# Optimization experiments

Measured on AMD Instinct MI355X. Metric: run time of the kernel, lower is better.

## Reference

```python
import jax, jax.numpy as jnp
import numpy as np

N = 50000      # nodes
E = 800000     # edges
H = 4          # heads (all layers)
D = 64         # per-head out dim (n_hidden == n_classes == 64)
IN = 256       # in_feats; also H*D so identity residual is valid
NEG_SLOPE = 0.2


def setup_inputs() -> dict:
    key = jax.random.key(0)
    ks = jax.random.split(key, 16)
    x = jax.random.normal(ks[0], (N, IN), dtype=jnp.float32)
    src = jax.random.randint(ks[1], (E,), 0, N, dtype=jnp.int32)
    dst = jax.random.randint(ks[2], (E,), 0, N, dtype=jnp.int32)
    inp = {"x": x, "src": src, "dst": dst}
    fan_ins = [IN, H * D, H * D]  # layer input widths
    for i, fin in enumerate(fan_ins):
        s = 1.0 / np.sqrt(fin)
        inp[f"W{i}"] = jax.random.normal(ks[3 + 4 * i], (fin, H * D), dtype=jnp.float32) * s
        inp[f"al{i}"] = jax.random.normal(ks[4 + 4 * i], (H, D), dtype=jnp.float32) * s
        inp[f"ar{i}"] = jax.random.normal(ks[5 + 4 * i], (H, D), dtype=jnp.float32) * s
        inp[f"b{i}"] = jnp.zeros((H * D,), dtype=jnp.float32)
    return inp


def _gat_layer(h, src, dst, W, al, ar, b, residual, activate):
    # project: [N, in] @ [in, H*D] -> [N, H, D]
    feat = (h @ W).reshape(-1, H, D)
    el = jnp.sum(feat * al, axis=-1)            # [N, H]
    er = jnp.sum(feat * ar, axis=-1)            # [N, H]
    e = jax.nn.leaky_relu(el[src] + er[dst], NEG_SLOPE)  # [E, H]
    # edge softmax per destination node (stable: subtract per-dst max)
    emax = jax.ops.segment_max(e, dst, num_segments=N)  # [N, H]
    e = jnp.exp(e - emax[dst])
    denom = jax.ops.segment_sum(e, dst, num_segments=N)  # [N, H]
    alpha = e / denom[dst]                               # [E, H]
    # message + scatter-aggregate: [E, H, D] summed into [N, H, D]
    out = jax.ops.segment_sum(alpha[:, :, None] * feat[src], dst, num_segments=N)
    if residual:
        out = out + h.reshape(-1, H, D)  # identity residual (in == H*D)
    out = out + b.reshape(1, H, D)
    if activate:
        out = jax.nn.elu(out)
    return out


def reference(x, src, dst, W0, al0, ar0, b0, W1, al1, ar1, b1, W2, al2, ar2, b2):
    h = _gat_layer(x, src, dst, W0, al0, ar0, b0, False, True).reshape(N, H * D)
    h = _gat_layer(h, src, dst, W1, al1, ar1, b1, True, True).reshape(N, H * D)
    h = _gat_layer(h, src, dst, W2, al2, ar2, b2, True, False).mean(axis=1)  # [N, D]
    return h
```

## Files before the change

kernel.cpp:

```cpp
#include <hip/hip_runtime.h>
#include <math.h>

#define N_NODES 50000
#define N_EDGES 800000
#define HD 256
#define NHEAD 4
#define DH 64
#define NPAD 50048

#define GEMM_BLKS 782
#define PACK_BLKS 96
#define EDGE_BLKS 1563
#define NB 49

typedef short bf16x8 __attribute__((ext_vector_type(8)));
typedef float f32x4 __attribute__((ext_vector_type(4)));

__device__ __forceinline__ unsigned short f2bf(float f) {
    unsigned u = __float_as_uint(f);
    return (unsigned short)((u + 0x7fffu + ((u >> 16) & 1u)) >> 16);
}
__device__ __forceinline__ float bf2f(unsigned short h) {
    return __uint_as_float((unsigned)h << 16);
}
__device__ __forceinline__ int origk(int k) {
    return (k & ~63) | ((k & 3) * 16 + ((k >> 2) & 15));
}

__device__ __forceinline__ void mfma_tile(const unsigned short* Asl,
                                          const unsigned short* wbase,
                                          int lane, f32x4 acc[4][4]) {
#pragma unroll
    for (int kk = 0; kk < 8; kk++) {
        bf16x8 a[4], b[4];
#pragma unroll
        for (int m = 0; m < 4; m++) {
            int r = m * 16 + (lane & 15);
            int kb = kk * 32 + (lane >> 4) * 8;
            int byt = (r * 512 + kb * 2) ^ ((r & 7) << 4);
            a[m] = *(const bf16x8*)((const char*)Asl + byt);
        }
#pragma unroll
        for (int n = 0; n < 4; n++)
            b[n] = *(const bf16x8*)(wbase + ((size_t)(n * 8 + kk) * 64 + lane) * 8);
#pragma unroll
        for (int m = 0; m < 4; m++)
#pragma unroll
            for (int n = 0; n < 4; n++)
                acc[m][n] = __builtin_amdgcn_mfma_f32_16x16x32_bf16(a[m], b[n],
                                                                    acc[m][n], 0, 0, 0);
    }
}

__device__ __forceinline__ void epilogue_tile(f32x4 acc[4][4], int bm, int wv, int lane,
                                              const float* __restrict__ al,
                                              const float* __restrict__ ar,
                                              unsigned short* __restrict__ C,
                                              unsigned short* __restrict__ el,
                                              float* __restrict__ er, int M) {
    int rr = lane >> 4, cc = lane & 15;
    float alv[4], arv[4];
#pragma unroll
    for (int n = 0; n < 4; n++) {
        alv[n] = al[wv * 64 + n * 16 + cc];
        arv[n] = ar[wv * 64 + n * 16 + cc];
    }
    float vl[16], vr[16];
#pragma unroll
    for (int m = 0; m < 4; m++)
#pragma unroll
        for (int r = 0; r < 4; r++) {
            float ep = 0.f, rp = 0.f;
#pragma unroll
            for (int n = 0; n < 4; n++) {
                ep = fmaf(acc[m][n][r], alv[n], ep);
                rp = fmaf(acc[m][n][r], arv[n], rp);
            }
            vl[m * 4 + r] = ep;
            vr[m * 4 + r] = rp;
        }
    float l8[8], r8[8];
#pragma unroll
    for (int i = 0; i < 8; i++) {
        float xs = (cc & 1) ? vl[2 * i] : vl[2 * i + 1];
        float xk = (cc & 1) ? vl[2 * i + 1] : vl[2 * i];
        l8[i] = xk + __shfl_xor(xs, 1);
        float ys = (cc & 1) ? vr[2 * i] : vr[2 * i + 1];
        float yk = (cc & 1) ? vr[2 * i + 1] : vr[2 * i];
        r8[i] = yk + __shfl_xor(ys, 1);
    }
    float l4[4], r4[4];
#pragma unroll
    for (int i = 0; i < 4; i++) {
        float xs = (cc & 2) ? l8[2 * i] : l8[2 * i + 1];
        float xk = (cc & 2) ? l8[2 * i + 1] : l8[2 * i];
        l4[i] = xk + __shfl_xor(xs, 2);
        float ys = (cc & 2) ? r8[2 * i] : r8[2 * i + 1];
        float yk = (cc & 2) ? r8[2 * i + 1] : r8[2 * i];
        r4[i] = yk + __shfl_xor(ys, 2);
    }
    float l2[2], r2[2];
#pragma unroll
    for (int i = 0; i < 2; i++) {
        float xs = (cc & 4) ? l4[2 * i] : l4[2 * i + 1];
        float xk = (cc & 4) ? l4[2 * i + 1] : l4[2 * i];
        l2[i] = xk + __shfl_xor(xs, 4);
        float ys = (cc & 4) ? r4[2 * i] : r4[2 * i + 1];
        float yk = (cc & 4) ? r4[2 * i + 1] : r4[2 * i];
        r2[i] = yk + __shfl_xor(ys, 4);
    }
    {
        float xs = (cc & 8) ? l2[0] : l2[1];
        float xk = (cc & 8) ? l2[1] : l2[0];
        float lv = xk + __shfl_xor(xs, 8);
        float ys = (cc & 8) ? r2[0] : r2[1];
        float yk = (cc & 8) ? r2[1] : r2[0];
        float rv = yk + __shfl_xor(ys, 8);
        int row_e = bm + (cc >> 2) * 16 + rr * 4 + (cc & 3);
        if (row_e < M) {
            el[(size_t)row_e * NHEAD + wv] = f2bf(lv);
            er[(size_t)row_e * NHEAD + wv] = rv;
        }
    }
#pragma unroll
    for (int m = 0; m < 4; m++) {
#pragma unroll
        for (int r = 0; r < 4; r++) {
            int row = bm + m * 16 + rr * 4 + r;
            if (row < M) {
                unsigned short p4[4] = {f2bf(acc[m][0][r]), f2bf(acc[m][1][r]),
                                        f2bf(acc[m][2][r]), f2bf(acc[m][3][r])};
                *(ushort4*)(C + (size_t)row * 256 + wv * 64 + cc * 4) = *(ushort4*)p4;
            }
        }
    }
}

__global__ __launch_bounds__(256) void fused_ph_k(const float* __restrict__ W0,
                                                  const float* __restrict__ W1,
                                                  const float* __restrict__ W2,
                                                  unsigned short* __restrict__ Wp,
                                                  const int* __restrict__ dst,
                                                  int* __restrict__ deg,
                                                  int* __restrict__ rank) {
    int blk = blockIdx.x, tid = threadIdx.x, wv = tid >> 6, lane = tid & 63;
    if (blk < PACK_BLKS) {
        int tile = blk * 4 + wv;
        int L = tile >> 7, t = tile & 127;
        const float* W = L == 0 ? W0 : L == 1 ? W1 : W2;
        int nt = t >> 3, kt = t & 7;
        int col = nt * 16 + (lane & 15);
        int kb = kt * 32 + (lane >> 4) * 8;
        unsigned short v[8];
#pragma unroll
        for (int j = 0; j < 8; j++) {
            int k = kb + j;
            if (L > 0) k = origk(k);
            v[j] = f2bf(W[(size_t)k * 256 + col]);
        }
        *(bf16x8*)(Wp + ((size_t)(L * 128 + t) * 64 + lane) * 8) = *(bf16x8*)v;
    } else {
        int t = (blk - PACK_BLKS) * 256 + tid;
        int e = t * 2;
        int* mydeg = deg + (size_t)(tid & 3) * NPAD;
        if (e + 1 < N_EDGES) {
            int2 d2 = *(const int2*)(dst + e);
            int r0 = atomicAdd(&mydeg[d2.x], 1);
            int r1 = atomicAdd(&mydeg[d2.y], 1);
            *(int2*)(rank + e) = make_int2(r0, r1);
        } else if (e < N_EDGES) {
            rank[e] = atomicAdd(&mydeg[dst[e]], 1);
        }
    }
}

__global__ __launch_bounds__(256) void scan1_k(const int* __restrict__ deg,
                                               int* __restrict__ rowptr,
                                               int* __restrict__ bsum,
                                               int* __restrict__ cpyoff) {
    __shared__ int wsum2[4];
    int tid = threadIdx.x, lane = tid & 63, wv = tid >> 6;
    int i0 = blockIdx.x * 1024 + tid * 4;
    int v[4], p[4];
#pragma unroll
    for (int j = 0; j < 4; j++) {
        int i = i0 + j;
        if (i < N_NODES) {
            int c0 = deg[i], c1 = deg[i + NPAD];
            int c2 = deg[i + 2 * NPAD], c3 = deg[i + 3 * NPAD];
            v[j] = c0 + c1 + c2 + c3;
            cpyoff[i] = 0;
            cpyoff[i + NPAD] = c0;
            cpyoff[i + 2 * NPAD] = c0 + c1;
            cpyoff[i + 3 * NPAD] = c0 + c1 + c2;
        } else {
            v[j] = 0;
        }
    }
    p[0] = v[0]; p[1] = p[0] + v[1]; p[2] = p[1] + v[2]; p[3] = p[2] + v[3];
    int tot = p[3];
    int sc = tot;
#pragma unroll
    for (int o = 1; o < 64; o <<= 1) {
        int t = __shfl_up(sc, o);
        if (lane >= o) sc += t;
    }
    if (lane == 63) wsum2[wv] = sc;
    __syncthreads();
    int woff = 0;
#pragma unroll
    for (int w = 0; w < 4; w++)
        if (w < wv) woff += wsum2[w];
    int excl = woff + sc - tot;
#pragma unroll
    for (int j = 0; j < 4; j++) {
        int i = i0 + j;
        if (i < N_NODES) rowptr[i + 1] = excl + p[j];
    }
    if (tid == 255) bsum[blockIdx.x] = excl + p[3];
}

__global__ __launch_bounds__(1024) void scan3_k(int* __restrict__ rowptr,
                                                const int* __restrict__ bsum, int nb) {
    __shared__ int boff_s;
    int tid = threadIdx.x;
    if (tid < 64) {
        int v = (tid < nb) ? bsum[tid] : 0;
        int sc = v;
#pragma unroll
        for (int o = 1; o < 64; o <<= 1) {
            int t = __shfl_up(sc, o);
            if ((tid & 63) >= o) sc += t;
        }
        if (tid == (int)blockIdx.x) boff_s = sc - v;
    }
    __syncthreads();
    int off = boff_s;
    int i = blockIdx.x * 1024 + tid;
    if (blockIdx.x == 0 && tid == 0) rowptr[0] = 0;
    if (i < N_NODES) rowptr[i + 1] += off;
}

__global__ __launch_bounds__(256) void fused_gsc_k(const float* __restrict__ A,
                                                   const unsigned short* __restrict__ Wp,
                                                   const float* __restrict__ al,
                                                   const float* __restrict__ ar,
                                                   unsigned short* __restrict__ C,
                                                   unsigned short* __restrict__ el,
                                                   float* __restrict__ er,
                                                   const int* __restrict__ src,
                                                   const int* __restrict__ dst,
                                                   const int* __restrict__ rank,
                                                   const int* __restrict__ rowptr,
                                                   const int* __restrict__ cpyoff,
                                                   int* __restrict__ csr_src, int M) {
    __shared__ unsigned short Asl[64 * 256];
    int blk = blockIdx.x, tid = threadIdx.x, wv = tid >> 6, lane = tid & 63;
    if (blk < GEMM_BLKS) {
        int bm = blk * 64;
#pragma unroll
        for (int i = 0; i < 8; i++) {
            int chunk = i * 256 + tid;
            int r = chunk >> 5, kc = (chunk & 31) * 8;
            float4 f0, f1;
            if (bm + r < M) {
                const float* p = A + (size_t)(bm + r) * 256 + kc;
                f0 = *(const float4*)p;
                f1 = *(const float4*)(p + 4);
            } else {
                f0 = f1 = make_float4(0.f, 0.f, 0.f, 0.f);
            }
            unsigned short tmp[8] = {f2bf(f0.x), f2bf(f0.y), f2bf(f0.z), f2bf(f0.w),
                                     f2bf(f1.x), f2bf(f1.y), f2bf(f1.z), f2bf(f1.w)};
            int b = (r * 512 + kc * 2) ^ ((r & 7) << 4);
            *(bf16x8*)((char*)Asl + b) = *(bf16x8*)tmp;
        }
        __syncthreads();
        const unsigned short* wbase = Wp + (size_t)(wv * 4) * 8 * 64 * 8;
        f32x4 acc[4][4] = {};
        mfma_tile(Asl, wbase, lane, acc);
        epilogue_tile(acc, bm, wv, lane, al, ar, C, el, er, M);
    } else {
        int t = (blk - GEMM_BLKS) * 256 + tid;
        int e = t * 2;
        const int* myoff = cpyoff + (size_t)(tid & 3) * NPAD;
        if (e + 1 < N_EDGES) {
            int2 s2 = *(const int2*)(src + e);
            int2 d2 = *(const int2*)(dst + e);
            int2 r2 = *(const int2*)(rank + e);
            csr_src[rowptr[d2.x] + myoff[d2.x] + r2.x] = s2.x;
            csr_src[rowptr[d2.y] + myoff[d2.y] + r2.y] = s2.y;
        } else if (e < N_EDGES) {
            int d = dst[e];
            csr_src[rowptr[d] + myoff[d] + rank[e]] = src[e];
        }
    }
}

__global__ __launch_bounds__(256) void gemm2_k(const unsigned short* __restrict__ A,
                                               const unsigned short* __restrict__ Wp,
                                               const float* __restrict__ al,
                                               const float* __restrict__ ar,
                                               unsigned short* __restrict__ C,
                                               unsigned short* __restrict__ el,
                                               float* __restrict__ er, int M) {
    __shared__ unsigned short Asl[2][64 * 256];
    int tid = threadIdx.x, wv = tid >> 6, lane = tid & 63;
    int bm0 = blockIdx.x * 128, bm1 = bm0 + 64;
#pragma unroll
    for (int i = 0; i < 8; i++) {
        int chunk = i * 256 + tid;
        int r = chunk >> 5;
        int c16 = (chunk & 31) ^ (r & 7);
        int grow = bm0 + r; if (grow >= M) grow = M - 1;
        __builtin_amdgcn_global_load_lds(
            (const __attribute__((address_space(1))) unsigned int*)
                (A + (size_t)grow * 256 + c16 * 8),
            (__attribute__((address_space(3))) unsigned int*)
                ((char*)Asl[0] + (size_t)chunk * 16),
            16, 0, 0);
    }
#pragma unroll
    for (int i = 0; i < 8; i++) {
        int chunk = i * 256 + tid;
        int r = chunk >> 5;
        int c16 = (chunk & 31) ^ (r & 7);
        int grow = bm1 + r; if (grow >= M) grow = M - 1;
        __builtin_amdgcn_global_load_lds(
            (const __attribute__((address_space(1))) unsigned int*)
                (A + (size_t)grow * 256 + c16 * 8),
            (__attribute__((address_space(3))) unsigned int*)
                ((char*)Asl[1] + (size_t)chunk * 16),
            16, 0, 0);
    }
    asm volatile("s_waitcnt vmcnt(8)" ::: "memory");
    __builtin_amdgcn_sched_barrier(0);
    __builtin_amdgcn_s_barrier();
    const unsigned short* wbase = Wp + (size_t)(wv * 4) * 8 * 64 * 8;
    f32x4 acc[4][4] = {};
    mfma_tile(Asl[0], wbase, lane, acc);
    asm volatile("s_waitcnt vmcnt(0)" ::: "memory");
    __builtin_amdgcn_sched_barrier(0);
    __builtin_amdgcn_s_barrier();
    epilogue_tile(acc, bm0, wv, lane, al, ar, C, el, er, M);
    f32x4 acc2[4][4] = {};
    mfma_tile(Asl[1], wbase, lane, acc2);
    epilogue_tile(acc2, bm1, wv, lane, al, ar, C, el, er, M);
}

template <int MODE>
__global__ __launch_bounds__(256) void agg_k(const int* __restrict__ rowptr,
                                             const int* __restrict__ csr_src,
                                             const unsigned short* __restrict__ el,
                                             const float* __restrict__ er,
                                             const unsigned short* __restrict__ feat,
                                             const unsigned short* __restrict__ resid,
                                             const float* __restrict__ bias,
                                             float* __restrict__ out,
                                             unsigned short* __restrict__ hb) {
    __shared__ int   ws_s[4][64];
    __shared__ float ws_w[4][4][68];
    int wv = threadIdx.x >> 6, lane = threadIdx.x & 63;
    int node = blockIdx.x * 4 + wv;
    if (node >= N_NODES) return;
    int beg = rowptr[node], end = rowptr[node + 1];
    float4 er4 = *(const float4*)(er + (size_t)node * 4);
    float4 acc0 = make_float4(0.f, 0.f, 0.f, 0.f);
    float4 acc1 = make_float4(0.f, 0.f, 0.f, 0.f);
    float4 den = make_float4(0.f, 0.f, 0.f, 0.f);
    int h = lane >> 4;
    int l8 = lane * 8;
    const char* fb = (const char*)feat;
    for (int base = beg; base < end; base += 64) {
        int j = base + lane;
        int soff = 0;
        float4 w = make_float4(0.f, 0.f, 0.f, 0.f);
        if (j < end) {
            int s = csr_src[j];
            soff = s << 9;
            ushort4 l4u = *(const ushort4*)(el + (size_t)s * 4);
            float vx = bf2f(l4u.x) + er4.x; vx = vx > 0.f ? vx : 0.2f * vx;
            float vy = bf2f(l4u.y) + er4.y; vy = vy > 0.f ? vy : 0.2f * vy;
            float vz = bf2f(l4u.z) + er4.z; vz = vz > 0.f ? vz : 0.2f * vz;
            float vw = bf2f(l4u.w) + er4.w; vw = vw > 0.f ? vw : 0.2f * vw;
            w.x = expf(vx); w.y = expf(vy); w.z = expf(vz); w.w = expf(vw);
            den.x += w.x; den.y += w.y; den.z += w.z; den.w += w.w;
        }
        ws_s[wv][lane] = soff;
        ws_w[wv][0][lane] = w.x;
        ws_w[wv][1][lane] = w.y;
        ws_w[wv][2][lane] = w.z;
        ws_w[wv][3][lane] = w.w;
        __builtin_amdgcn_wave_barrier();
        int cnt = end - base; if (cnt > 64) cnt = 64;
        int cnt4 = (cnt + 3) & ~3;
        for (int k = 0; k < cnt4; k += 4) {
            int4   so = *(const int4*)&ws_s[wv][k];
            float4 w4 = *(const float4*)&ws_w[wv][h][k];
            ushort4 u0 = *(const ushort4*)(fb + (so.x + l8));
            ushort4 u1 = *(const ushort4*)(fb + (so.y + l8));
            ushort4 u2 = *(const ushort4*)(fb + (so.z + l8));
            ushort4 u3 = *(const ushort4*)(fb + (so.w + l8));
            acc0.x = fmaf(w4.x, bf2f(u0.x), acc0.x);
            acc0.y = fmaf(w4.x, bf2f(u0.y), acc0.y);
            acc0.z = fmaf(w4.x, bf2f(u0.z), acc0.z);
            acc0.w = fmaf(w4.x, bf2f(u0.w), acc0.w);
            acc1.x = fmaf(w4.y, bf2f(u1.x), acc1.x);
            acc1.y = fmaf(w4.y, bf2f(u1.y), acc1.y);
            acc1.z = fmaf(w4.y, bf2f(u1.z), acc1.z);
            acc1.w = fmaf(w4.y, bf2f(u1.w), acc1.w);
            acc0.x = fmaf(w4.z, bf2f(u2.x), acc0.x);
            acc0.y = fmaf(w4.z, bf2f(u2.y), acc0.y);
            acc0.z = fmaf(w4.z, bf2f(u2.z), acc0.z);
            acc0.w = fmaf(w4.z, bf2f(u2.w), acc0.w);
            acc1.x = fmaf(w4.w, bf2f(u3.x), acc1.x);
            acc1.y = fmaf(w4.w, bf2f(u3.y), acc1.y);
            acc1.z = fmaf(w4.w, bf2f(u3.z), acc1.z);
            acc1.w = fmaf(w4.w, bf2f(u3.w), acc1.w);
        }
        __builtin_amdgcn_wave_barrier();
    }
    float4 acc;
    acc.x = acc0.x + acc1.x; acc.y = acc0.y + acc1.y;
    acc.z = acc0.z + acc1.z; acc.w = acc0.w + acc1.w;
#pragma unroll
    for (int o = 1; o < 64; o <<= 1) {
        den.x += __shfl_xor(den.x, o);
        den.y += __shfl_xor(den.y, o);
        den.z += __shfl_xor(den.z, o);
        den.w += __shfl_xor(den.w, o);
    }
    float den_me = h == 0 ? den.x : h == 1 ? den.y : h == 2 ? den.z : den.w;
    float r = den_me > 0.f ? 1.f / den_me : 0.f;
    int cc = lane & 15;
    float4 b4;
    b4.x = bias[h * 64 + 0 * 16 + cc];
    b4.y = bias[h * 64 + 1 * 16 + cc];
    b4.z = bias[h * 64 + 2 * 16 + cc];
    b4.w = bias[h * 64 + 3 * 16 + cc];
    float4 o4;
    o4.x = acc.x * r + b4.x;
    o4.y = acc.y * r + b4.y;
    o4.z = acc.z * r + b4.z;
    o4.w = acc.w * r + b4.w;
    if (MODE >= 1) {
        ushort4 r4 = *(const ushort4*)(resid + (size_t)node * HD + lane * 4);
        o4.x += bf2f(r4.x); o4.y += bf2f(r4.y);
        o4.z += bf2f(r4.z); o4.w += bf2f(r4.w);
    }
    if (MODE <= 1) {
        o4.x = o4.x > 0.f ? o4.x : expm1f(o4.x);
        o4.y = o4.y > 0.f ? o4.y : expm1f(o4.y);
        o4.z = o4.z > 0.f ? o4.z : expm1f(o4.z);
        o4.w = o4.w > 0.f ? o4.w : expm1f(o4.w);
        ushort4 hv;
        hv.x = f2bf(o4.x); hv.y = f2bf(o4.y); hv.z = f2bf(o4.z); hv.w = f2bf(o4.w);
        *(ushort4*)(hb + (size_t)node * HD + lane * 4) = hv;
    } else {
        o4.x += __shfl_xor(o4.x, 16); o4.x += __shfl_xor(o4.x, 32);
        o4.y += __shfl_xor(o4.y, 16); o4.y += __shfl_xor(o4.y, 32);
        o4.z += __shfl_xor(o4.z, 16); o4.z += __shfl_xor(o4.z, 32);
        o4.w += __shfl_xor(o4.w, 16); o4.w += __shfl_xor(o4.w, 32);
        if (lane < 16) {
            float* po = out + (size_t)node * DH;
            po[0 * 16 + lane] = o4.x * 0.25f;
            po[1 * 16 + lane] = o4.y * 0.25f;
            po[2 * 16 + lane] = o4.z * 0.25f;
            po[3 * 16 + lane] = o4.w * 0.25f;
        }
    }
}

extern "C" void kernel_launch(void* const* d_in, const int* in_sizes, int n_in,
                              void* d_out, int out_size, void* d_ws, size_t ws_size,
                              hipStream_t stream) {
    const float* x   = (const float*)d_in[0];
    const int*   src = (const int*)d_in[1];
    const int*   dst = (const int*)d_in[2];
    const float* W[3]  = {(const float*)d_in[3], (const float*)d_in[7],  (const float*)d_in[11]};
    const float* al[3] = {(const float*)d_in[4], (const float*)d_in[8],  (const float*)d_in[12]};
    const float* ar[3] = {(const float*)d_in[5], (const float*)d_in[9],  (const float*)d_in[13]};
    const float* bb[3] = {(const float*)d_in[6], (const float*)d_in[10], (const float*)d_in[14]};

    size_t big = (size_t)N_NODES * HD;
    unsigned short* featb = (unsigned short*)d_ws;
    unsigned short* hb1 = featb + big;
    unsigned short* hb2 = hb1 + big;
    unsigned short* el = hb2 + big;
    float* er = (float*)(el + (size_t)NPAD * NHEAD);
    int* deg     = (int*)(er + (size_t)NPAD * NHEAD);
    int* cpyoff  = deg + 4 * NPAD;
    int* rowptr  = cpyoff + 4 * NPAD;
    int* rank    = rowptr + NPAD;
    int* csr_src = rank + N_EDGES;
    int* bsum    = csr_src + N_EDGES;
    unsigned short* Wp = (unsigned short*)(bsum + 64);

    hipMemsetAsync(deg, 0, (size_t)4 * NPAD * 4, stream);
    fused_ph_k<<<PACK_BLKS + EDGE_BLKS, 256, 0, stream>>>(W[0], W[1], W[2], Wp,
                                                          dst, deg, rank);
    scan1_k<<<NB, 256, 0, stream>>>(deg, rowptr, bsum, cpyoff);
    scan3_k<<<NB, 1024, 0, stream>>>(rowptr, bsum, NB);
    fused_gsc_k<<<GEMM_BLKS + EDGE_BLKS, 256, 0, stream>>>(
        x, Wp, al[0], ar[0], featb, el, er, src, dst, rank, rowptr, cpyoff,
        csr_src, N_NODES);

    int g2grid = (N_NODES + 127) / 128;
    int agrid = (N_NODES + 3) / 4;

    agg_k<0><<<agrid, 256, 0, stream>>>(rowptr, csr_src, el, er, featb,
                                        nullptr, bb[0], nullptr, hb1);
    gemm2_k<<<g2grid, 256, 0, stream>>>(hb1, Wp + (size_t)1 * 128 * 64 * 8,
                                        al[1], ar[1], featb, el, er, N_NODES);
    agg_k<1><<<agrid, 256, 0, stream>>>(rowptr, csr_src, el, er, featb,
                                        hb1, bb[1], nullptr, hb2);
    gemm2_k<<<g2grid, 256, 0, stream>>>(hb2, Wp + (size_t)2 * 128 * 64 * 8,
                                        al[2], ar[2], featb, el, er, N_NODES);
    agg_k<2><<<agrid, 256, 0, stream>>>(rowptr, csr_src, el, er, featb,
                                        hb2, bb[2], (float*)d_out, nullptr);
}
```

Measured before the change: 296.9 us.

## Fold scan3 into fused GEMM/scatter kernel using block-local scatter bases

Removes the separate scan3 launch. scan1 now writes per-copy local start offsets (sbase) instead of cpyoff. Each block of the fused kernel recomputes the block-sum exclusive scan into LDS, so scatter blocks read one base per destination instead of rowptr plus cpyoff, and extra tail blocks finalize rowptr. This saves one kernel launch and a dependent global pass, at the cost of a small redundant 64-lane scan in every edge block.

Result: no change. 293.9 us (-1.0%).

```diff
diff --git a/kernel.cpp b/kernel.cpp
--- a/kernel.cpp
+++ b/kernel.cpp
@@ -177,11 +177,11 @@
 __global__ __launch_bounds__(256) void scan1_k(const int* __restrict__ deg,
                                                int* __restrict__ rowptr,
                                                int* __restrict__ bsum,
-                                               int* __restrict__ cpyoff) {
+                                               int* __restrict__ sbase) {
     __shared__ int wsum2[4];
     int tid = threadIdx.x, lane = tid & 63, wv = tid >> 6;
     int i0 = blockIdx.x * 1024 + tid * 4;
-    int v[4], p[4];
+    int v[4], p[4], c0s[4], c1s[4], c2s[4];
 #pragma unroll
     for (int j = 0; j < 4; j++) {
         int i = i0 + j;
@@ -189,12 +189,9 @@
             int c0 = deg[i], c1 = deg[i + NPAD];
             int c2 = deg[i + 2 * NPAD], c3 = deg[i + 3 * NPAD];
             v[j] = c0 + c1 + c2 + c3;
-            cpyoff[i] = 0;
-            cpyoff[i + NPAD] = c0;
-            cpyoff[i + 2 * NPAD] = c0 + c1;
-            cpyoff[i + 3 * NPAD] = c0 + c1 + c2;
+            c0s[j] = c0; c1s[j] = c1; c2s[j] = c2;
         } else {
-            v[j] = 0;
+            v[j] = 0; c0s[j] = c1s[j] = c2s[j] = 0;
         }
     }
     p[0] = v[0]; p[1] = p[0] + v[1]; p[2] = p[1] + v[2]; p[3] = p[2] + v[3];
@@ -215,33 +212,35 @@
 #pragma unroll
     for (int j = 0; j < 4; j++) {
         int i = i0 + j;
-        if (i < N_NODES) rowptr[i + 1] = excl + p[j];
+        if (i < N_NODES) {
+            int incl = excl + p[j];
+            rowptr[i + 1] = incl;
+            int start = incl - v[j];
+            sbase[i] = start;
+            sbase[i + NPAD] = start + c0s[j];
+            sbase[i + 2 * NPAD] = start + c0s[j] + c1s[j];
+            sbase[i + 3 * NPAD] = start + c0s[j] + c1s[j] + c2s[j];
+        }
     }
     if (tid == 255) bsum[blockIdx.x] = excl + p[3];
 }
 
-__global__ __launch_bounds__(1024) void scan3_k(int* __restrict__ rowptr,
-                                                const int* __restrict__ bsum, int nb) {
-    __shared__ int boff_s;
-    int tid = threadIdx.x;
+__device__ __forceinline__ void boff_to_lds(const int* __restrict__ bsum,
+                                            int* __restrict__ boffs, int tid) {
     if (tid < 64) {
-        int v = (tid < nb) ? bsum[tid] : 0;
+        int v = (tid < NB) ? bsum[tid] : 0;
         int sc = v;
 #pragma unroll
         for (int o = 1; o < 64; o <<= 1) {
             int t = __shfl_up(sc, o);
             if ((tid & 63) >= o) sc += t;
         }
-        if (tid == (int)blockIdx.x) boff_s = sc - v;
+        boffs[tid] = sc - v;
     }
     __syncthreads();
-    int off = boff_s;
-    int i = blockIdx.x * 1024 + tid;
-    if (blockIdx.x == 0 && tid == 0) rowptr[0] = 0;
-    if (i < N_NODES) rowptr[i + 1] += off;
-}
-
-__global__ __launch_bounds__(256) void fused_gsc_k(const float* __restrict__ A,
+}
+
+__global__ __launch_bounds__(256) void fused_gsf_k(const float* __restrict__ A,
                                                    const unsigned short* __restrict__ Wp,
                                                    const float* __restrict__ al,
                                                    const float* __restrict__ ar,
@@ -251,8 +250,9 @@
                                                    const int* __restrict__ src,
                                                    const int* __restrict__ dst,
                                                    const int* __restrict__ rank,
-                                                   const int* __restrict__ rowptr,
-                                                   const int* __restrict__ cpyoff,
+                                                   int* __restrict__ rowptr,
+                                                   const int* __restrict__ sbase,
+                                                   const int* __restrict__ bsum,
                                                    int* __restrict__ csr_src, int M) {
     __shared__ unsigned short Asl[64 * 256];
     int blk = blockIdx.x, tid = threadIdx.x, wv = tid >> 6, lane = tid & 63;
@@ -280,19 +280,33 @@
         f32x4 acc[4][4] = {};
         mfma_tile(Asl, wbase, lane, acc);
         epilogue_tile(acc, bm, wv, lane, al, ar, C, el, er, M);
-    } else {
+    } else if (blk < GEMM_BLKS + EDGE_BLKS) {
+        int* boffs = (int*)Asl;
+        boff_to_lds(bsum, boffs, tid);
         int t = (blk - GEMM_BLKS) * 256 + tid;
         int e = t * 2;
-        const int* myoff = cpyoff + (size_t)(tid & 3) * NPAD;
+        const int* mybase = sbase + (size_t)(tid & 3) * NPAD;
         if (e + 1 < N_EDGES) {
             int2 s2 = *(const int2*)(src + e);
             int2 d2 = *(const int2*)(dst + e);
             int2 r2 = *(const int2*)(rank + e);
-            csr_src[rowptr[d2.x] + myoff[d2.x] + r2.x] = s2.x;
-            csr_src[rowptr[d2.y] + myoff[d2.y] + r2.y] = s2.y;
+            csr_src[mybase[d2.x] + boffs[d2.x >> 10] + r2.x] = s2.x;
+            csr_src[mybase[d2.y] + boffs[d2.y >> 10] + r2.y] = s2.y;
         } else if (e < N_EDGES) {
             int d = dst[e];
-            csr_src[rowptr[d] + myoff[d] + rank[e]] = src[e];
+            csr_src[mybase[d] + boffs[d >> 10] + rank[e]] = src[e];
+        }
+    } else {
+        int* boffs = (int*)Asl;
+        boff_to_lds(bsum, boffs, tid);
+        int sblk = blk - GEMM_BLKS - EDGE_BLKS;
+        int off = boffs[sblk];
+        int i0 = sblk * 1024 + tid * 4;
+        if (sblk == 0 && tid == 0) rowptr[0] = 0;
+#pragma unroll
+        for (int j = 0; j < 4; j++) {
+            int i = i0 + j;
+            if (i < N_NODES) rowptr[i + 1] += off;
         }
     }
 }
@@ -489,8 +503,8 @@
     unsigned short* el = hb2 + big;
     float* er = (float*)(el + (size_t)NPAD * NHEAD);
     int* deg     = (int*)(er + (size_t)NPAD * NHEAD);
-    int* cpyoff  = deg + 4 * NPAD;
-    int* rowptr  = cpyoff + 4 * NPAD;
+    int* sbase   = deg + 4 * NPAD;
+    int* rowptr  = sbase + 4 * NPAD;
     int* rank    = rowptr + NPAD;
     int* csr_src = rank + N_EDGES;
     int* bsum    = csr_src + N_EDGES;
@@ -499,10 +513,9 @@
     hipMemsetAsync(deg, 0, (size_t)4 * NPAD * 4, stream);
     fused_ph_k<<<PACK_BLKS + EDGE_BLKS, 256, 0, stream>>>(W[0], W[1], W[2], Wp,
                                                           dst, deg, rank);
-    scan1_k<<<NB, 256, 0, stream>>>(deg, rowptr, bsum, cpyoff);
-    scan3_k<<<NB, 1024, 0, stream>>>(rowptr, bsum, NB);
-    fused_gsc_k<<<GEMM_BLKS + EDGE_BLKS, 256, 0, stream>>>(
-        x, Wp, al[0], ar[0], featb, el, er, src, dst, rank, rowptr, cpyoff,
+    scan1_k<<<NB, 256, 0, stream>>>(deg, rowptr, bsum, sbase);
+    fused_gsf_k<<<GEMM_BLKS + EDGE_BLKS + NB, 256, 0, stream>>>(
+        x, Wp, al[0], ar[0], featb, el, er, src, dst, rank, rowptr, sbase, bsum,
         csr_src, N_NODES);
 
     int g2grid = (N_NODES + 127) / 128;
```
